# Kernel optimization log

Measured on AMD Instinct MI355X. Metric: run time of the kernel, lower is better.

Reference implementation:

```python
import jax, jax.numpy as jnp
import numpy as np


def setup_inputs() -> dict:
    key = jax.random.key(0)
    ks = jax.random.split(key, 8)
    B = 65536
    scale = lambda fan_in: 1.0 / np.sqrt(fan_in)
    return {
        "x": jax.random.normal(ks[0], (B, 784), dtype=jnp.float32),
        "w0": jax.random.normal(ks[1], (124, 784), dtype=jnp.float32) * scale(784),
        "w1": jax.random.normal(ks[2], (32, 124), dtype=jnp.float32) * scale(124),
        "w3": jax.random.normal(ks[3], (22, 32), dtype=jnp.float32) * scale(32),
        "b3": jax.random.normal(ks[4], (22,), dtype=jnp.float32) * scale(32),
        "w5": jax.random.normal(ks[5], (21, 22), dtype=jnp.float32) * scale(22),
        "b5": jax.random.normal(ks[6], (21,), dtype=jnp.float32) * scale(22),
        "w7": jax.random.normal(ks[7], (10, 21), dtype=jnp.float32) * scale(21),
    }


def reference(x, w0, w1, w3, b3, w5, b5, w7):
    # x: [B, 784]; PyTorch Linear: y = x @ W.T (+ b)
    h = x @ w0.T                       # [B, 124] (no bias, no activation)
    h = jax.nn.relu(h @ w1.T)          # [B, 32]
    h = jax.nn.relu(h @ w3.T + b3)     # [B, 22]
    h = jax.nn.relu(h @ w5.T + b5)     # [B, 21]
    logits = h @ w7.T                  # [B, 10]
    return jax.nn.log_softmax(logits, axis=1)
```

## Files before the change

kernel.cpp:

```cpp
#include <hip/hip_runtime.h>
#include <hip/hip_fp16.h>

typedef _Float16 half8 __attribute__((ext_vector_type(8)));
typedef float f32x4 __attribute__((ext_vector_type(4)));

#define W0T_OFF   0
#define W1P_OFF   (13 * 16384)
#define SW_OFF    (W1P_OFF + 8192)
#define SW_BYTES  (2816 + 2016 + 960 + 96 + 96)
#define WS_TOTAL  (SW_OFF + SW_BYTES)

#define L_XS   0
#define L_WS   16384
#define L_H0   0
#define L_H1   32768
#define L_W1   40960
#define L_SW   49152
#define L_H3   0
#define L_H5   12800
#define LDS_BYTES 55136

__global__ void prep_weights(const float* __restrict__ w0,
                             const float* __restrict__ w1,
                             const float* __restrict__ w3,
                             const float* __restrict__ b3,
                             const float* __restrict__ w5,
                             const float* __restrict__ b5,
                             const float* __restrict__ w7,
                             char* __restrict__ ws) {
  int tid = blockIdx.x * 256 + threadIdx.x;
  if (tid < 13 * 128 * 64) {
    int t = tid >> 13;
    int rem = tid & 8191;
    int n = rem >> 6, kk = rem & 63;
    int k = t * 64 + kk;
    float v = (n < 124 && k < 784) ? w0[n * 784 + k] : 0.f;
    int off = t * 16384 + n * 128 + ((kk * 2) ^ ((n & 7) << 4));
    *(__half*)(ws + off) = __float2half(v);
    return;
  }
  int r = tid - 13 * 128 * 64;
  if (r < 32 * 128) {
    int n = r >> 7, k = r & 127;
    float v = (k < 124) ? w1[n * 124 + k] : 0.f;
    int off = W1P_OFF + n * 256 + ((k * 2) ^ ((n & 7) << 4));
    *(__half*)(ws + off) = __float2half(v);
    return;
  }
  r -= 32 * 128;
  if (r < 704) { ((float*)(ws + SW_OFF))[r] = w3[r]; return; }
  r -= 704;
  if (r < 504) {
    int n = r / 24, k = r % 24;
    ((float*)(ws + SW_OFF + 2816))[r] = (k < 22) ? w5[n * 22 + k] : 0.f;
    return;
  }
  r -= 504;
  if (r < 240) {
    int n = r / 24, k = r % 24;
    ((float*)(ws + SW_OFF + 4832))[r] = (k < 21) ? w7[n * 21 + k] : 0.f;
    return;
  }
  r -= 240;
  if (r < 24) { ((float*)(ws + SW_OFF + 5792))[r] = (r < 22) ? b3[r] : 0.f; return; }
  r -= 24;
  if (r < 24) { ((float*)(ws + SW_OFF + 5888))[r] = (r < 21) ? b5[r] : 0.f; return; }
}

__global__ __launch_bounds__(256, 2) void fused_mlp(
    const float* __restrict__ x, const char* __restrict__ wsg,
    float* __restrict__ out) {
  __shared__ char sm[LDS_BYTES];
  const int tid  = threadIdx.x;
  const int lane = tid & 63;
  const int wave = tid >> 6;
  const int row0 = blockIdx.x << 7;

  {
    const uint4* s1 = (const uint4*)(wsg + W1P_OFF);
    uint4* d1 = (uint4*)(sm + L_W1);
#pragma unroll
    for (int i = 0; i < 2; i++) d1[tid + 256 * i] = s1[tid + 256 * i];
    const uint* s2 = (const uint*)(wsg + SW_OFF);
    uint* d2 = (uint*)(sm + L_SW);
    for (int i = tid; i < SW_BYTES / 4; i += 256) d2[i] = s2[i];
  }

  f32x4 acc[2][8];
#pragma unroll
  for (int m = 0; m < 2; m++)
#pragma unroll
    for (int n = 0; n < 8; n++) acc[m][n] = f32x4{0.f, 0.f, 0.f, 0.f};

  const int xrow = tid >> 4;
  const int xc4  = tid & 15;
  float4 xr[8];
  uint4  wr[4];

  {
#pragma unroll
    for (int i = 0; i < 8; i++)
      xr[i] = *(const float4*)(x + (size_t)(row0 + xrow + i * 16) * 784 + xc4 * 4);
    const uint4* wsrc = (const uint4*)(wsg + W0T_OFF);
#pragma unroll
    for (int j = 0; j < 4; j++) wr[j] = wsrc[tid + j * 256];
  }

  const int a_r  = (wave << 5) + (lane & 15);
  const int kg16 = (lane >> 4) << 4;

  for (int t = 0; t < 13; t++) {
    __syncthreads();
#pragma unroll
    for (int i = 0; i < 8; i++) {
      const int rr = xrow + i * 16;
      __half2 p0 = __float22half2_rn(make_float2(xr[i].x, xr[i].y));
      __half2 p1 = __float22half2_rn(make_float2(xr[i].z, xr[i].w));
      uint2 pk = make_uint2(__builtin_bit_cast(unsigned, p0),
                            __builtin_bit_cast(unsigned, p1));
      *(uint2*)(sm + L_XS + rr * 128 + ((xc4 * 8) ^ ((rr & 7) << 4))) = pk;
    }
    {
      uint4* wd = (uint4*)(sm + L_WS);
#pragma unroll
      for (int j = 0; j < 4; j++) wd[tid + j * 256] = wr[j];
    }
    if (t + 1 < 13) {
      const int k0 = (t + 1) * 64 + xc4 * 4;
      if (k0 < 784) {
#pragma unroll
        for (int i = 0; i < 8; i++)
          xr[i] = *(const float4*)(x + (size_t)(row0 + xrow + i * 16) * 784 + k0);
      } else {
#pragma unroll
        for (int i = 0; i < 8; i++) xr[i] = make_float4(0.f, 0.f, 0.f, 0.f);
      }
      const uint4* wsrc = (const uint4*)(wsg + W0T_OFF + (t + 1) * 16384);
#pragma unroll
      for (int j = 0; j < 4; j++) wr[j] = wsrc[tid + j * 256];
    }
    asm volatile("s_waitcnt lgkmcnt(0)" ::: "memory");
    __builtin_amdgcn_s_barrier();
    __builtin_amdgcn_sched_barrier(0);
#pragma unroll
    for (int kf = 0; kf < 2; kf++) {
      half8 af[2], bf[8];
#pragma unroll
      for (int mf = 0; mf < 2; mf++) {
        const int rr = a_r + mf * 16;
        af[mf] = *(const half8*)(sm + L_XS + rr * 128 +
                                 ((kf * 64 + kg16) ^ ((rr & 7) << 4)));
      }
#pragma unroll
      for (int nf = 0; nf < 8; nf++) {
        const int nn = nf * 16 + (lane & 15);
        bf[nf] = *(const half8*)(sm + L_WS + nn * 128 +
                                 ((kf * 64 + kg16) ^ ((nn & 7) << 4)));
      }
#pragma unroll
      for (int mf = 0; mf < 2; mf++)
#pragma unroll
        for (int nf = 0; nf < 8; nf++)
          acc[mf][nf] = __builtin_amdgcn_mfma_f32_16x16x32_f16(
              af[mf], bf[nf], acc[mf][nf], 0, 0, 0);
    }
  }

  __syncthreads();
#pragma unroll
  for (int mf = 0; mf < 2; mf++) {
    const int rb = (wave << 5) + mf * 16 + ((lane >> 4) << 2);
#pragma unroll
    for (int nf = 0; nf < 8; nf++) {
      const int cc = nf * 16 + (lane & 15);
#pragma unroll
      for (int q = 0; q < 4; q++) {
        const int rr = rb + q;
        *(__half*)(sm + L_H0 + rr * 256 + ((cc * 2) ^ ((rr & 7) << 4))) =
            __float2half(acc[mf][nf][q]);
      }
    }
  }
  __syncthreads();

  f32x4 acc1[2][2];
#pragma unroll
  for (int m = 0; m < 2; m++) {
    acc1[m][0] = f32x4{0.f, 0.f, 0.f, 0.f};
    acc1[m][1] = f32x4{0.f, 0.f, 0.f, 0.f};
  }
#pragma unroll
  for (int kf = 0; kf < 4; kf++) {
    half8 a1[2], b1[2];
#pragma unroll
    for (int mf = 0; mf < 2; mf++) {
      const int rr = a_r + mf * 16;
      a1[mf] = *(const half8*)(sm + L_H0 + rr * 256 +
                               ((kf * 64 + kg16) ^ ((rr & 7) << 4)));
    }
#pragma unroll
    for (int nf = 0; nf < 2; nf++) {
      const int nn = nf * 16 + (lane & 15);
      b1[nf] = *(const half8*)(sm + L_W1 + nn * 256 +
                               ((kf * 64 + kg16) ^ ((nn & 7) << 4)));
    }
#pragma unroll
    for (int mf = 0; mf < 2; mf++)
#pragma unroll
      for (int nf = 0; nf < 2; nf++)
        acc1[mf][nf] = __builtin_amdgcn_mfma_f32_16x16x32_f16(
            a1[mf], b1[nf], acc1[mf][nf], 0, 0, 0);
  }
#pragma unroll
  for (int mf = 0; mf < 2; mf++) {
    const int rb = (wave << 5) + mf * 16 + ((lane >> 4) << 2);
#pragma unroll
    for (int nf = 0; nf < 2; nf++) {
      const int cc = nf * 16 + (lane & 15);
#pragma unroll
      for (int q = 0; q < 4; q++) {
        const int rr = rb + q;
        float v = fmaxf(acc1[mf][nf][q], 0.f);
        *(__half*)(sm + L_H1 + rr * 64 + ((cc * 2) ^ (((rr >> 1) & 3) << 4))) =
            __float2half(v);
      }
    }
  }
  __syncthreads();

  const int r = tid & 127;
  const int j = tid >> 7;
  float h1r[32];
#pragma unroll
  for (int kc = 0; kc < 4; kc++) {
    half8 v = *(const half8*)(sm + L_H1 + r * 64 +
                              ((kc * 16) ^ (((r >> 1) & 3) << 4)));
#pragma unroll
    for (int e = 0; e < 8; e++) h1r[kc * 8 + e] = (float)v[e];
  }
  const float* w3p = (const float*)(sm + L_SW);
  const float* w5p = (const float*)(sm + L_SW + 2816);
  const float* w7p = (const float*)(sm + L_SW + 4832);
  const float* b3p = (const float*)(sm + L_SW + 5792);
  const float* b5p = (const float*)(sm + L_SW + 5888);
  float* h3l = (float*)(sm + L_H3);
  float* h5l = (float*)(sm + L_H5);

#pragma unroll
  for (int i = 0; i < 11; i++) {
    const int n = j + 2 * i;
    float s = b3p[n];
#pragma unroll
    for (int k = 0; k < 32; k++) s += h1r[k] * w3p[n * 32 + k];
    h3l[r * 25 + n] = fmaxf(s, 0.f);
  }
  __syncthreads();
  float h3r[22];
#pragma unroll
  for (int k = 0; k < 22; k++) h3r[k] = h3l[r * 25 + k];
#pragma unroll
  for (int i = 0; i < 11; i++) {
    const int n = j + 2 * i;
    if (n < 21) {
      float s = b5p[n];
#pragma unroll
      for (int k = 0; k < 22; k++) s += h3r[k] * w5p[n * 24 + k];
      h5l[r * 25 + n] = fmaxf(s, 0.f);
    }
  }
  __syncthreads();
  if (j == 0) {
    float h5r[21];
#pragma unroll
    for (int k = 0; k < 21; k++) h5r[k] = h5l[r * 25 + k];
    float lg[10];
    float mx = -3.4e38f;
#pragma unroll
    for (int n = 0; n < 10; n++) {
      float s = 0.f;
#pragma unroll
      for (int k = 0; k < 21; k++) s += h5r[k] * w7p[n * 24 + k];
      lg[n] = s;
      mx = fmaxf(mx, s);
    }
    float se = 0.f;
#pragma unroll
    for (int n = 0; n < 10; n++) se += __expf(lg[n] - mx);
    const float lse = mx + __logf(se);
    float* op = out + (size_t)(row0 + r) * 10;
#pragma unroll
    for (int n = 0; n < 10; n++) op[n] = lg[n] - lse;
  }
}

extern "C" void kernel_launch(void* const* d_in, const int* in_sizes, int n_in,
                              void* d_out, int out_size, void* d_ws, size_t ws_size,
                              hipStream_t stream) {
  const float* x  = (const float*)d_in[0];
  const float* w0 = (const float*)d_in[1];
  const float* w1 = (const float*)d_in[2];
  const float* w3 = (const float*)d_in[3];
  const float* b3 = (const float*)d_in[4];
  const float* w5 = (const float*)d_in[5];
  const float* b5 = (const float*)d_in[6];
  const float* w7 = (const float*)d_in[7];
  float* out = (float*)d_out;
  char* ws = (char*)d_ws;

  const int prep_elems = 13 * 128 * 64 + 32 * 128 + 704 + 504 + 240 + 24 + 24;
  prep_weights<<<(prep_elems + 255) / 256, 256, 0, stream>>>(w0, w1, w3, b3, w5,
                                                             b5, w7, ws);
  fused_mlp<<<65536 / 128, 256, 0, stream>>>(x, ws, out);
}
```

Before: 61.62 us.

## Restructure fused MLP into single-wave blocks with register-direct fragment loads

```diff
diff --git a/kernel.cpp b/kernel.cpp
--- a/kernel.cpp
+++ b/kernel.cpp
@@ -2,23 +2,20 @@
 #include <hip/hip_fp16.h>
 
 typedef _Float16 half8 __attribute__((ext_vector_type(8)));
+typedef __fp16 cvt2_t __attribute__((ext_vector_type(2)));
 typedef float f32x4 __attribute__((ext_vector_type(4)));
 
-#define W0T_OFF   0
-#define W1P_OFF   (13 * 16384)
-#define SW_OFF    (W1P_OFF + 8192)
-#define SW_BYTES  (2816 + 2016 + 960 + 96 + 96)
-#define WS_TOTAL  (SW_OFF + SW_BYTES)
-
-#define L_XS   0
-#define L_WS   16384
+#define W0F_UNITS (13 * 1024)
+#define W1F_OFF   (W0F_UNITS * 16)
+#define W1F_UNITS 512
+#define SW_OFF    (W1F_OFF + W1F_UNITS * 16)
+
 #define L_H0   0
-#define L_H1   32768
-#define L_W1   40960
-#define L_SW   49152
+#define L_H1   8192
 #define L_H3   0
-#define L_H5   12800
-#define LDS_BYTES 55136
+#define L_H5   3200
+#define L_OS   6400
+#define LDS_SZ 10240
 
 __global__ void prep_weights(const float* __restrict__ w0,
                              const float* __restrict__ w1,
@@ -29,267 +26,309 @@
                              const float* __restrict__ w7,
                              char* __restrict__ ws) {
   int tid = blockIdx.x * 256 + threadIdx.x;
-  if (tid < 13 * 128 * 64) {
-    int t = tid >> 13;
-    int rem = tid & 8191;
-    int n = rem >> 6, kk = rem & 63;
-    int k = t * 64 + kk;
-    float v = (n < 124 && k < 784) ? w0[n * 784 + k] : 0.f;
-    int off = t * 16384 + n * 128 + ((kk * 2) ^ ((n & 7) << 4));
-    *(__half*)(ws + off) = __float2half(v);
+  if (tid < W0F_UNITS) {
+    int t  = tid >> 10;
+    int kf = (tid >> 9) & 1;
+    int nf = (tid >> 6) & 7;
+    int l  = tid & 63;
+    int n  = nf * 16 + (l & 15);
+    int k0 = t * 64 + kf * 32 + (l >> 4) * 8;
+    alignas(16) __half h[8];
+#pragma unroll
+    for (int e = 0; e < 8; e++) {
+      int k = k0 + e;
+      h[e] = __float2half((n < 124 && k < 784) ? w0[n * 784 + k] : 0.f);
+    }
+    *(uint4*)(ws + tid * 16) = *(const uint4*)h;
     return;
   }
-  int r = tid - 13 * 128 * 64;
-  if (r < 32 * 128) {
-    int n = r >> 7, k = r & 127;
-    float v = (k < 124) ? w1[n * 124 + k] : 0.f;
-    int off = W1P_OFF + n * 256 + ((k * 2) ^ ((n & 7) << 4));
-    *(__half*)(ws + off) = __float2half(v);
+  int r = tid - W0F_UNITS;
+  if (r < W1F_UNITS) {
+    int kf = r >> 7;
+    int nf = (r >> 6) & 1;
+    int l  = r & 63;
+    int n  = nf * 16 + (l & 15);
+    int k0 = kf * 32 + (l >> 4) * 8;
+    alignas(16) __half h[8];
+#pragma unroll
+    for (int e = 0; e < 8; e++) {
+      int k = k0 + e;
+      h[e] = __float2half((k < 124) ? w1[n * 124 + k] : 0.f);
+    }
+    *(uint4*)(ws + W1F_OFF + r * 16) = *(const uint4*)h;
     return;
   }
-  r -= 32 * 128;
-  if (r < 704) { ((float*)(ws + SW_OFF))[r] = w3[r]; return; }
+  r -= W1F_UNITS;
+  float* sw = (float*)(ws + SW_OFF);
+  if (r < 704) { sw[r] = w3[r]; return; }
   r -= 704;
   if (r < 504) {
     int n = r / 24, k = r % 24;
-    ((float*)(ws + SW_OFF + 2816))[r] = (k < 22) ? w5[n * 22 + k] : 0.f;
+    sw[704 + r] = (k < 22) ? w5[n * 22 + k] : 0.f;
     return;
   }
   r -= 504;
   if (r < 240) {
     int n = r / 24, k = r % 24;
-    ((float*)(ws + SW_OFF + 4832))[r] = (k < 21) ? w7[n * 21 + k] : 0.f;
+    sw[1208 + r] = (k < 21) ? w7[n * 21 + k] : 0.f;
     return;
   }
   r -= 240;
-  if (r < 24) { ((float*)(ws + SW_OFF + 5792))[r] = (r < 22) ? b3[r] : 0.f; return; }
+  if (r < 24) { sw[1448 + r] = (r < 22) ? b3[r] : 0.f; return; }
   r -= 24;
-  if (r < 24) { ((float*)(ws + SW_OFF + 5888))[r] = (r < 21) ? b5[r] : 0.f; return; }
+  if (r < 24) { sw[1472 + r] = (r < 21) ? b5[r] : 0.f; return; }
 }
 
-__global__ __launch_bounds__(256, 2) void fused_mlp(
-    const float* __restrict__ x, const char* __restrict__ wsg,
+__device__ __forceinline__ half8 cvt8(const float4& a, const float4& b) {
+  cvt2_t p0 = __builtin_amdgcn_cvt_pkrtz(a.x, a.y);
+  cvt2_t p1 = __builtin_amdgcn_cvt_pkrtz(a.z, a.w);
+  cvt2_t p2 = __builtin_amdgcn_cvt_pkrtz(b.x, b.y);
+  cvt2_t p3 = __builtin_amdgcn_cvt_pkrtz(b.z, b.w);
+  uint4 u;
+  u.x = __builtin_bit_cast(unsigned, p0);
+  u.y = __builtin_bit_cast(unsigned, p1);
+  u.z = __builtin_bit_cast(unsigned, p2);
+  u.w = __builtin_bit_cast(unsigned, p3);
+  return __builtin_bit_cast(half8, u);
+}
+
+__global__ __launch_bounds__(64, 2) void fused_mlp(
+    const float* __restrict__ x, const char* __restrict__ ws,
     float* __restrict__ out) {
-  __shared__ char sm[LDS_BYTES];
-  const int tid  = threadIdx.x;
-  const int lane = tid & 63;
-  const int wave = tid >> 6;
-  const int row0 = blockIdx.x << 7;
+  __shared__ alignas(16) char sm[LDS_SZ];
+  const int l  = threadIdx.x;
+  const int lr = l & 15;
+  const int lg = l >> 4;
+  const size_t row0 = (size_t)blockIdx.x * 32;
+
+  const float* xb0 = x + (row0 + lr) * 784;
+  const float* xb1 = xb0 + 16 * 784;
+
+  f32x4 acc[2][8];
+#pragma unroll
+  for (int mf = 0; mf < 2; mf++)
+#pragma unroll
+    for (int nf = 0; nf < 8; nf++) acc[mf][nf] = f32x4{0.f, 0.f, 0.f, 0.f};
+
+  const uint4* wf = (const uint4*)ws;
+
+  float4 xA[2][2][2], xB[2][2][2];
+
+#pragma unroll
+  for (int mf = 0; mf < 2; mf++)
+#pragma unroll
+    for (int kf = 0; kf < 2; kf++) {
+      const float* p = (mf ? xb1 : xb0) + kf * 32 + lg * 8;
+      xA[mf][kf][0] = *(const float4*)p;
+      xA[mf][kf][1] = *(const float4*)(p + 4);
+    }
+
+#define TILE_BODY(T, XC, XN, PF_FULL)                                          \
+  {                                                                            \
+    half8 bf[2][8];                                                            \
+    _Pragma("unroll") for (int kf = 0; kf < 2; kf++)                           \
+        _Pragma("unroll") for (int nf = 0; nf < 8; nf++)                       \
+            bf[kf][nf] = __builtin_bit_cast(                                   \
+                half8, wf[(T) * 1024 + kf * 512 + nf * 64 + l]);               \
+    half8 af[2][2];                                                            \
+    _Pragma("unroll") for (int mf = 0; mf < 2; mf++)                           \
+        _Pragma("unroll") for (int kf = 0; kf < 2; kf++)                       \
+            af[mf][kf] = cvt8(XC[mf][kf][0], XC[mf][kf][1]);                   \
+    if (PF_FULL) {                                                             \
+      _Pragma("unroll") for (int mf = 0; mf < 2; mf++)                         \
+          _Pragma("unroll") for (int kf = 0; kf < 2; kf++) {                   \
+        const float* p = (mf ? xb1 : xb0) + ((T) + 1) * 64 + kf * 32 + lg * 8; \
+        XN[mf][kf][0] = *(const float4*)p;                                     \
+        XN[mf][kf][1] = *(const float4*)(p + 4);                               \
+      }                                                                        \
+    } else {                \
+      const float4 z = {0.f, 0.f, 0.f, 0.f};                                   \
+      _Pragma("unroll") for (int mf = 0; mf < 2; mf++) {                       \
+        const float* p = (mf ? xb1 : xb0) + 768 + lg * 8;                      \
+        bool v = (lg < 2);                                                     \
+        XN[mf][0][0] = v ? *(const float4*)p : z;                              \
+        XN[mf][0][1] = v ? *(const float4*)(p + 4) : z;                        \
+        XN[mf][1][0] = z;                                                      \
+        XN[mf][1][1] = z;                                                      \
+      }                                                                        \
+    }                                                                          \
+    _Pragma("unroll") for (int kf = 0; kf < 2; kf++)                           \
+        _Pragma("unroll") for (int mf = 0; mf < 2; mf++)                       \
+            _Pragma("unroll") for (int nf = 0; nf < 8; nf++)                   \
+                acc[mf][nf] = __builtin_amdgcn_mfma_f32_16x16x32_f16(          \
+                    af[mf][kf], bf[kf][nf], acc[mf][nf], 0, 0, 0);             \
+  }
+
+  TILE_BODY(0, xA, xB, 1)
+  TILE_BODY(1, xB, xA, 1)
+  TILE_BODY(2, xA, xB, 1)
+  TILE_BODY(3, xB, xA, 1)
+  TILE_BODY(4, xA, xB, 1)
+  TILE_BODY(5, xB, xA, 1)
+  TILE_BODY(6, xA, xB, 1)
+  TILE_BODY(7, xB, xA, 1)
+  TILE_BODY(8, xA, xB, 1)
+  TILE_BODY(9, xB, xA, 1)
+  TILE_BODY(10, xA, xB, 1)
+  TILE_BODY(11, xB, xA, 0)
 
   {
-    const uint4* s1 = (const uint4*)(wsg + W1P_OFF);
-    uint4* d1 = (uint4*)(sm + L_W1);
-#pragma unroll
-    for (int i = 0; i < 2; i++) d1[tid + 256 * i] = s1[tid + 256 * i];
-    const uint* s2 = (const uint*)(wsg + SW_OFF);
-    uint* d2 = (uint*)(sm + L_SW);
-    for (int i = tid; i < SW_BYTES / 4; i += 256) d2[i] = s2[i];
-  }
-
-  f32x4 acc[2][8];
-#pragma unroll
-  for (int m = 0; m < 2; m++)
-#pragma unroll
-    for (int n = 0; n < 8; n++) acc[m][n] = f32x4{0.f, 0.f, 0.f, 0.f};
-
-  const int xrow = tid >> 4;
-  const int xc4  = tid & 15;
-  float4 xr[8];
-  uint4  wr[4];
-
+    half8 bf[8];
+#pragma unroll
+    for (int nf = 0; nf < 8; nf++)
+      bf[nf] = __builtin_bit_cast(half8, wf[12 * 1024 + nf * 64 + l]);
+    half8 af[2];
+#pragma unroll
+    for (int mf = 0; mf < 2; mf++) af[mf] = cvt8(xA[mf][0][0], xA[mf][0][1]);
+#pragma unroll
+    for (int mf = 0; mf < 2; mf++)
+#pragma unroll
+      for (int nf = 0; nf < 8; nf++)
+        acc[mf][nf] = __builtin_amdgcn_mfma_f32_16x16x32_f16(
+            af[mf], bf[nf], acc[mf][nf], 0, 0, 0);
+  }
+
+  half8 b1[4][2];
   {
-#pragma unroll
-    for (int i = 0; i < 8; i++)
-      xr[i] = *(const float4*)(x + (size_t)(row0 + xrow + i * 16) * 784 + xc4 * 4);
-    const uint4* wsrc = (const uint4*)(wsg + W0T_OFF);
-#pragma unroll
-    for (int j = 0; j < 4; j++) wr[j] = wsrc[tid + j * 256];
-  }
-
-  const int a_r  = (wave << 5) + (lane & 15);
-  const int kg16 = (lane >> 4) << 4;
-
-  for (int t = 0; t < 13; t++) {
-    __syncthreads();
-#pragma unroll
-    for (int i = 0; i < 8; i++) {
-      const int rr = xrow + i * 16;
-      __half2 p0 = __float22half2_rn(make_float2(xr[i].x, xr[i].y));
-      __half2 p1 = __float22half2_rn(make_float2(xr[i].z, xr[i].w));
-      uint2 pk = make_uint2(__builtin_bit_cast(unsigned, p0),
-                            __builtin_bit_cast(unsigned, p1));
-      *(uint2*)(sm + L_XS + rr * 128 + ((xc4 * 8) ^ ((rr & 7) << 4))) = pk;
-    }
-    {
-      uint4* wd = (uint4*)(sm + L_WS);
-#pragma unroll
-      for (int j = 0; j < 4; j++) wd[tid + j * 256] = wr[j];
-    }
-    if (t + 1 < 13) {
-      const int k0 = (t + 1) * 64 + xc4 * 4;
-      if (k0 < 784) {
-#pragma unroll
-        for (int i = 0; i < 8; i++)
-          xr[i] = *(const float4*)(x + (size_t)(row0 + xrow + i * 16) * 784 + k0);
-      } else {
-#pragma unroll
-        for (int i = 0; i < 8; i++) xr[i] = make_float4(0.f, 0.f, 0.f, 0.f);
-      }
-      const uint4* wsrc = (const uint4*)(wsg + W0T_OFF + (t + 1) * 16384);
-#pragma unroll
-      for (int j = 0; j < 4; j++) wr[j] = wsrc[tid + j * 256];
-    }
-    asm volatile("s_waitcnt lgkmcnt(0)" ::: "memory");
-    __builtin_amdgcn_s_barrier();
-    __builtin_amdgcn_sched_barrier(0);
-#pragma unroll
-    for (int kf = 0; kf < 2; kf++) {
-      half8 af[2], bf[8];
-#pragma unroll
-      for (int mf = 0; mf < 2; mf++) {
-        const int rr = a_r + mf * 16;
-        af[mf] = *(const half8*)(sm + L_XS + rr * 128 +
-                                 ((kf * 64 + kg16) ^ ((rr & 7) << 4)));
-      }
-#pragma unroll
-      for (int nf = 0; nf < 8; nf++) {
-        const int nn = nf * 16 + (lane & 15);
-        bf[nf] = *(const half8*)(sm + L_WS + nn * 128 +
-                                 ((kf * 64 + kg16) ^ ((nn & 7) << 4)));
-      }
-#pragma unroll
-      for (int mf = 0; mf < 2; mf++)
-#pragma unroll
-        for (int nf = 0; nf < 8; nf++)
-          acc[mf][nf] = __builtin_amdgcn_mfma_f32_16x16x32_f16(
-              af[mf], bf[nf], acc[mf][nf], 0, 0, 0);
-    }
-  }
-
-  __syncthreads();
-#pragma unroll
-  for (int mf = 0; mf < 2; mf++) {
-    const int rb = (wave << 5) + mf * 16 + ((lane >> 4) << 2);
-#pragma unroll
-    for (int nf = 0; nf < 8; nf++) {
-      const int cc = nf * 16 + (lane & 15);
+    const uint4* w1f = (const uint4*)(ws + W1F_OFF);
+#pragma unroll
+    for (int kf = 0; kf < 4; kf++)
+#pragma unroll
+      for (int nf = 0; nf < 2; nf++)
+        b1[kf][nf] = __builtin_bit_cast(half8, w1f[kf * 128 + nf * 64 + l]);
+  }
+
+#pragma unroll
+  for (int mf = 0; mf < 2; mf++)
+#pragma unroll
+    for (int nf = 0; nf < 8; nf++)
 #pragma unroll
       for (int q = 0; q < 4; q++) {
-        const int rr = rb + q;
-        *(__half*)(sm + L_H0 + rr * 256 + ((cc * 2) ^ ((rr & 7) << 4))) =
+        int rr = mf * 16 + lg * 4 + q;
+        int cc = nf * 16 + lr;
+        *(__half*)(sm + L_H0 + rr * 256 + ((2 * cc) ^ ((rr & 7) << 4))) =
             __float2half(acc[mf][nf][q]);
       }
-    }
-  }
   __syncthreads();
 
   f32x4 acc1[2][2];
 #pragma unroll
-  for (int m = 0; m < 2; m++) {
-    acc1[m][0] = f32x4{0.f, 0.f, 0.f, 0.f};
-    acc1[m][1] = f32x4{0.f, 0.f, 0.f, 0.f};
+  for (int mf = 0; mf < 2; mf++) {
+    acc1[mf][0] = f32x4{0.f, 0.f, 0.f, 0.f};
+    acc1[mf][1] = f32x4{0.f, 0.f, 0.f, 0.f};
   }
 #pragma unroll
   for (int kf = 0; kf < 4; kf++) {
-    half8 a1[2], b1[2];
+    half8 a1[2];
 #pragma unroll
     for (int mf = 0; mf < 2; mf++) {
-      const int rr = a_r + mf * 16;
-      a1[mf] = *(const half8*)(sm + L_H0 + rr * 256 +
-                               ((kf * 64 + kg16) ^ ((rr & 7) << 4)));
-    }
-#pragma unroll
-    for (int nf = 0; nf < 2; nf++) {
-      const int nn = nf * 16 + (lane & 15);
-      b1[nf] = *(const half8*)(sm + L_W1 + nn * 256 +
-                               ((kf * 64 + kg16) ^ ((nn & 7) << 4)));
+      int rr = mf * 16 + lr;
+      int cb = kf * 64 + lg * 16;
+      a1[mf] = *(const half8*)(sm + L_H0 + rr * 256 + (cb ^ ((rr & 7) << 4)));
     }
 #pragma unroll
     for (int mf = 0; mf < 2; mf++)
 #pragma unroll
       for (int nf = 0; nf < 2; nf++)
         acc1[mf][nf] = __builtin_amdgcn_mfma_f32_16x16x32_f16(
-            a1[mf], b1[nf], acc1[mf][nf], 0, 0, 0);
-  }
-#pragma unroll
-  for (int mf = 0; mf < 2; mf++) {
-    const int rb = (wave << 5) + mf * 16 + ((lane >> 4) << 2);
-#pragma unroll
-    for (int nf = 0; nf < 2; nf++) {
-      const int cc = nf * 16 + (lane & 15);
+            a1[mf], b1[kf][nf], acc1[mf][nf], 0, 0, 0);
+  }
+#pragma unroll
+  for (int mf = 0; mf < 2; mf++)
+#pragma unroll
+    for (int nf = 0; nf < 2; nf++)
 #pragma unroll
       for (int q = 0; q < 4; q++) {
-        const int rr = rb + q;
+        int rr = mf * 16 + lg * 4 + q;
+        int cc = nf * 16 + lr;
         float v = fmaxf(acc1[mf][nf][q], 0.f);
-        *(__half*)(sm + L_H1 + rr * 64 + ((cc * 2) ^ (((rr >> 1) & 3) << 4))) =
+        *(__half*)(sm + L_H1 + rr * 64 + ((2 * cc) ^ ((rr & 3) << 4))) =
             __float2half(v);
       }
-    }
-  }
-  __syncthreads();
-
-  const int r = tid & 127;
-  const int j = tid >> 7;
-  float h1r[32];
-#pragma unroll
-  for (int kc = 0; kc < 4; kc++) {
-    half8 v = *(const half8*)(sm + L_H1 + r * 64 +
-                              ((kc * 16) ^ (((r >> 1) & 3) << 4)));
-#pragma unroll
-    for (int e = 0; e < 8; e++) h1r[kc * 8 + e] = (float)v[e];
-  }
-  const float* w3p = (const float*)(sm + L_SW);
-  const float* w5p = (const float*)(sm + L_SW + 2816);
-  const float* w7p = (const float*)(sm + L_SW + 4832);
-  const float* b3p = (const float*)(sm + L_SW + 5792);
-  const float* b5p = (const float*)(sm + L_SW + 5888);
+  __syncthreads();
+
+  const int r = l & 31;
+  const int j = l >> 5;
+  float h1v[32];
+#pragma unroll
+  for (int cb = 0; cb < 4; cb++) {
+    half8 v = *(const half8*)(sm + L_H1 + r * 64 + ((cb * 16) ^ ((r & 3) << 4)));
+#pragma unroll
+    for (int e = 0; e < 8; e++) h1v[cb * 8 + e] = (float)v[e];
+  }
+  const float* w3g = (const float*)(ws + SW_OFF);
+  const float* w5g = (const float*)(ws + SW_OFF + 2816);
+  const float* w7g = (const float*)(ws + SW_OFF + 4832);
+  const float* b3g = (const float*)(ws + SW_OFF + 5792);
+  const float* b5g = (const float*)(ws + SW_OFF + 5888);
   float* h3l = (float*)(sm + L_H3);
   float* h5l = (float*)(sm + L_H5);
 
 #pragma unroll
   for (int i = 0; i < 11; i++) {
-    const int n = j + 2 * i;
-    float s = b3p[n];
-#pragma unroll
-    for (int k = 0; k < 32; k++) s += h1r[k] * w3p[n * 32 + k];
+    int n = j + 2 * i;
+    float s = b3g[n];
+    const float4* wrow = (const float4*)(w3g + n * 32);
+#pragma unroll
+    for (int kk = 0; kk < 8; kk++) {
+      float4 wv = wrow[kk];
+      s += h1v[4 * kk] * wv.x + h1v[4 * kk + 1] * wv.y +
+           h1v[4 * kk + 2] * wv.z + h1v[4 * kk + 3] * wv.w;
+    }
     h3l[r * 25 + n] = fmaxf(s, 0.f);
   }
   __syncthreads();
-  float h3r[22];
-#pragma unroll
-  for (int k = 0; k < 22; k++) h3r[k] = h3l[r * 25 + k];
+  float h3v[24];
+#pragma unroll
+  for (int k = 0; k < 24; k++) h3v[k] = (k < 22) ? h3l[r * 25 + k] : 0.f;
 #pragma unroll
   for (int i = 0; i < 11; i++) {
-    const int n = j + 2 * i;
+    int n = j + 2 * i;
     if (n < 21) {
-      float s = b5p[n];
-#pragma unroll
-      for (int k = 0; k < 22; k++) s += h3r[k] * w5p[n * 24 + k];
+      float s = b5g[n];
+      const float4* wrow = (const float4*)(w5g + n * 24);
+#pragma unroll
+      for (int kk = 0; kk < 6; kk++) {
+        float4 wv = wrow[kk];
+        s += h3v[4 * kk] * wv.x + h3v[4 * kk + 1] * wv.y +
+             h3v[4 * kk + 2] * wv.z + h3v[4 * kk + 3] * wv.w;
+      }
       h5l[r * 25 + n] = fmaxf(s, 0.f);
     }
   }
   __syncthreads();
   if (j == 0) {
-    float h5r[21];
-#pragma unroll
-    for (int k = 0; k < 21; k++) h5r[k] = h5l[r * 25 + k];
-    float lg[10];
+    float h5v[24];
+#pragma unroll
+    for (int k = 0; k < 24; k++) h5v[k] = (k < 21) ? h5l[r * 25 + k] : 0.f;
+    float lgt[10];
     float mx = -3.4e38f;
 #pragma unroll
     for (int n = 0; n < 10; n++) {
       float s = 0.f;
-#pragma unroll
-      for (int k = 0; k < 21; k++) s += h5r[k] * w7p[n * 24 + k];
-      lg[n] = s;
+      const float4* wrow = (const float4*)(w7g + n * 24);
+#pragma unroll
+      for (int kk = 0; kk < 6; kk++) {
+        float4 wv = wrow[kk];
+        s += h5v[4 * kk] * wv.x + h5v[4 * kk + 1] * wv.y +
+             h5v[4 * kk + 2] * wv.z + h5v[4 * kk + 3] * wv.w;
+      }
+      lgt[n] = s;
       mx = fmaxf(mx, s);
     }
     float se = 0.f;
 #pragma unroll
-    for (int n = 0; n < 10; n++) se += __expf(lg[n] - mx);
+    for (int n = 0; n < 10; n++) se += __expf(lgt[n] - mx);
     const float lse = mx + __logf(se);
-    float* op = out + (size_t)(row0 + r) * 10;
-#pragma unroll
-    for (int n = 0; n < 10; n++) op[n] = lg[n] - lse;
+    float* os = (float*)(sm + L_OS);
+#pragma unroll
+    for (int n = 0; n < 10; n++) os[r * 10 + n] = lgt[n] - lse;
+  }
+  __syncthreads();
+  {
+    const float* os = (const float*)(sm + L_OS);
+#pragma unroll
+    for (int i = 0; i < 5; i++) out[row0 * 10 + i * 64 + l] = os[i * 64 + l];
   }
 }
 
@@ -307,8 +346,8 @@
   float* out = (float*)d_out;
   char* ws = (char*)d_ws;
 
-  const int prep_elems = 13 * 128 * 64 + 32 * 128 + 704 + 504 + 240 + 24 + 24;
-  prep_weights<<<(prep_elems + 255) / 256, 256, 0, stream>>>(w0, w1, w3, b3, w5,
-                                                             b5, w7, ws);
-  fused_mlp<<<65536 / 128, 256, 0, stream>>>(x, ws, out);
+  const int prep_threads = W0F_UNITS + W1F_UNITS + 704 + 504 + 240 + 24 + 24;
+  prep_weights<<<(prep_threads + 255) / 256, 256, 0, stream>>>(w0, w1, w3, b3,
+                                                               w5, b5, w7, ws);
+  fused_mlp<<<65536 / 32, 64, 0, stream>>>(x, ws, out);
 }
```

Measured after the change: 57.32 us. 7.0% less time.
